# Kernel tuning notes

Measured on AMD Instinct MI355X. Metric: run time of the kernel, lower is better.

The kernel has to match this reference:

```python
import math
import jax, jax.numpy as jnp
import numpy as np

B, S, H, N = 2, 2048, 2048, 16
HN = H // N
ALPHA = 32.0
MASK_VALUE = 10000.0


def setup_inputs() -> dict:
    key = jax.random.key(0)
    k1, k2, k3, k4, k5 = jax.random.split(key, 5)
    hidden_states = jax.random.normal(k1, (B, S, H), dtype=jnp.float32)
    # causal (left-to-right) multiplicative mask, broadcastable to [b, n, s, s]
    ltor_mask = jnp.tril(jnp.ones((S, S), dtype=jnp.float32))[None, None, :, :]
    # torch Linear params: y = x @ W.T + b
    w_qkv = jax.random.normal(k2, (3 * H, H), dtype=jnp.float32) * (1.0 / math.sqrt(H))
    b_qkv = jnp.zeros((3 * H,), dtype=jnp.float32)
    w_dense = jax.random.normal(k3, (H, H), dtype=jnp.float32) * (1.0 / math.sqrt(H))
    b_dense = jnp.zeros((H,), dtype=jnp.float32)
    return {"hidden_states": hidden_states, "ltor_mask": ltor_mask,
            "w_qkv": w_qkv, "b_qkv": b_qkv, "w_dense": w_dense, "b_dense": b_dense}


def reference(hidden_states, ltor_mask, w_qkv, b_qkv, w_dense, b_dense):
    b, s, h = hidden_states.shape
    # fused qkv projection
    qkv = hidden_states @ w_qkv.T + b_qkv                       # [b, s, 3h]
    q, k, v = jnp.split(qkv, 3, axis=-1)

    def heads(t):  # [b, s, h] -> [b, n, s, hn]
        return t.reshape(b, s, N, HN).transpose(0, 2, 1, 3)

    q, k, v = heads(q), heads(k), heads(v)
    # cogview pb_relax: scale query before matmul
    scores = jnp.einsum('bnsd,bntd->bnst', q / math.sqrt(HN), k)  # [b, n, s, s]
    m = ltor_mask[:, :, -s:]
    scores = scores * m - MASK_VALUE * (1.0 - m)
    # pb_relax max stabilization: per (batch, head) global max of scores/alpha
    scaled = scores / ALPHA
    maxes = jax.lax.stop_gradient(jnp.max(scaled, axis=(-2, -1), keepdims=True))
    scores = (scaled - maxes) * ALPHA
    probs = jax.nn.softmax(scores, axis=-1)
    ctx = jnp.einsum('bnst,bntd->bnsd', probs, v)                # [b, n, s, hn]
    ctx = ctx.transpose(0, 2, 1, 3).reshape(b, s, h)
    out = ctx @ w_dense.T + b_dense
    return out
```

## Files before the change

kernel.cpp:

```cpp
#include <hip/hip_runtime.h>

typedef __bf16 bf16_t;
typedef __bf16 bf16x8 __attribute__((ext_vector_type(8)));
typedef __bf16 bf16x4 __attribute__((ext_vector_type(4)));
typedef float f32x4 __attribute__((ext_vector_type(4)));

#define MFMA16(a, b, c) __builtin_amdgcn_mfma_f32_16x16x32_bf16((a), (b), (c), 0, 0, 0)

__device__ __forceinline__ void gload_lds16(const void* g, void* l) {
  __builtin_amdgcn_global_load_lds(
      (__attribute__((address_space(1))) void*)(g),
      (__attribute__((address_space(3))) void*)(l), 16, 0, 0);
}

__device__ __forceinline__ void block_bar() {
  asm volatile("" ::: "memory");
  __builtin_amdgcn_s_barrier();
  asm volatile("" ::: "memory");
}

__global__ __launch_bounds__(256) void cvt_f32_bf16(const float* __restrict__ in,
                                                    bf16_t* __restrict__ out, int n4) {
  int i = blockIdx.x * 256 + threadIdx.x;
  if (i >= n4) return;
  float4 v = ((const float4*)in)[i];
  bf16x4 o;
  o[0] = (bf16_t)v.x; o[1] = (bf16_t)v.y; o[2] = (bf16_t)v.z; o[3] = (bf16_t)v.w;
  ((bf16x4*)out)[i] = o;
}

__global__ __launch_bounds__(512) void gemm_qkv_256(
    const bf16_t* __restrict__ A, const bf16_t* __restrict__ Bw,
    const float* __restrict__ bias,
    bf16_t* __restrict__ qb, bf16_t* __restrict__ kb, bf16_t* __restrict__ vtb,
    int M, int N, int K) {
  __shared__ __attribute__((aligned(16))) bf16_t As[2][256][64];
  __shared__ __attribute__((aligned(16))) bf16_t Bs[2][256][64];
  const int tid = threadIdx.x;
  const int lane = tid & 63;
  const int w = tid >> 6;
  const int wm = w >> 2, wn = w & 3;
  const int l15 = lane & 15, l4 = lane >> 4;
  const int bm = blockIdx.y * 256, bn = blockIdx.x * 256;

  f32x4 acc[8][4];
#pragma unroll
  for (int i = 0; i < 8; ++i)
#pragma unroll
    for (int j = 0; j < 4; ++j)
#pragma unroll
      for (int r = 0; r < 4; ++r) acc[i][j][r] = 0.0f;

  const int srow = tid >> 3;
  const int schk = tid & 7;

  auto stageA = [&](int q, int ti, int i) {
    int r = (i << 6) + srow;
    int cl = (schk ^ (r & 7)) << 3;
    gload_lds16(A + (size_t)(bm + r) * K + (ti << 6) + cl, &As[q][r][schk << 3]);
  };
  auto stageB = [&](int q, int ti, int i) {
    int r = (i << 6) + srow;
    int cl = (schk ^ (r & 7)) << 3;
    gload_lds16(Bw + (size_t)(bn + r) * K + (ti << 6) + cl, &Bs[q][r][schk << 3]);
  };
  auto afrag = [&](int p, int mf, int ks) -> bf16x8 {
    int row = wm * 128 + mf * 16 + l15;
    int ch = ((ks << 2) | l4) ^ (row & 7);
    return *(const bf16x8*)(&As[p][row][ch << 3]);
  };
  auto bfrag = [&](int p, int nf, int ks) -> bf16x8 {
    int row = wn * 64 + nf * 16 + l15;
    int ch = ((ks << 2) | l4) ^ (row & 7);
    return *(const bf16x8*)(&Bs[p][row][ch << 3]);
  };

  const int nt = K >> 6;

#pragma unroll
  for (int i = 0; i < 4; ++i) stageA(0, 0, i);
#pragma unroll
  for (int i = 0; i < 4; ++i) stageB(0, 0, i);

  bf16x8 afr[4], bfr[4];

#pragma unroll 1
  for (int t = 0; t < nt; ++t) {
    const int p = t & 1, q = p ^ 1;
    const bool pf = (t + 1 < nt);
    asm volatile("s_waitcnt vmcnt(0)" ::: "memory");
    block_bar();

#pragma unroll
    for (int n = 0; n < 4; ++n) bfr[n] = bfrag(p, n, 0);
#pragma unroll
    for (int j = 0; j < 4; ++j) afr[j] = afrag(p, j, 0);
    if (pf) { stageA(q, t + 1, 0); stageA(q, t + 1, 1); }
    block_bar();
    __builtin_amdgcn_s_setprio(1);
#pragma unroll
    for (int j = 0; j < 4; ++j)
#pragma unroll
      for (int n = 0; n < 4; ++n) acc[j][n] = MFMA16(afr[j], bfr[n], acc[j][n]);
    __builtin_amdgcn_s_setprio(0);
    block_bar();

#pragma unroll
    for (int j = 0; j < 4; ++j) afr[j] = afrag(p, 4 + j, 0);
    if (pf) { stageA(q, t + 1, 2); stageA(q, t + 1, 3); }
    block_bar();
    __builtin_amdgcn_s_setprio(1);
#pragma unroll
    for (int j = 0; j < 4; ++j)
#pragma unroll
      for (int n = 0; n < 4; ++n) acc[4 + j][n] = MFMA16(afr[j], bfr[n], acc[4 + j][n]);
    __builtin_amdgcn_s_setprio(0);
    block_bar();

#pragma unroll
    for (int n = 0; n < 4; ++n) bfr[n] = bfrag(p, n, 1);
#pragma unroll
    for (int j = 0; j < 4; ++j) afr[j] = afrag(p, j, 1);
    if (pf) { stageB(q, t + 1, 0); stageB(q, t + 1, 1); }
    block_bar();
    __builtin_amdgcn_s_setprio(1);
#pragma unroll
    for (int j = 0; j < 4; ++j)
#pragma unroll
      for (int n = 0; n < 4; ++n) acc[j][n] = MFMA16(afr[j], bfr[n], acc[j][n]);
    __builtin_amdgcn_s_setprio(0);
    block_bar();

#pragma unroll
    for (int j = 0; j < 4; ++j) afr[j] = afrag(p, 4 + j, 1);
    if (pf) { stageB(q, t + 1, 2); stageB(q, t + 1, 3); }
    block_bar();
    __builtin_amdgcn_s_setprio(1);
#pragma unroll
    for (int j = 0; j < 4; ++j)
#pragma unroll
      for (int n = 0; n < 4; ++n) acc[4 + j][n] = MFMA16(afr[j], bfr[n], acc[4 + j][n]);
    __builtin_amdgcn_s_setprio(0);
    block_bar();
  }

  const int which = bn >> 11;
#pragma unroll
  for (int mf = 0; mf < 8; ++mf)
#pragma unroll
    for (int nf = 0; nf < 4; ++nf)
#pragma unroll
      for (int r = 0; r < 4; ++r) {
        int m = bm + wm * 128 + mf * 16 + l4 * 4 + r;
        int n = bn + wn * 64 + nf * 16 + l15;
        float v = acc[mf][nf][r] + bias[n];
        int b = m >> 11, s = m & 2047;
        int d = n & 127;
        int head = (n & 2047) >> 7;
        size_t hb = (size_t)(b * 16 + head);
        if (which == 0) {
          v *= 0.08838834764831845f;
          qb[(hb * 2048 + s) * 128 + d] = (bf16_t)v;
        } else if (which == 1) {
          kb[(hb * 2048 + s) * 128 + d] = (bf16_t)v;
        } else {
          vtb[(hb * 128 + d) * 2048 + s] = (bf16_t)v;
        }
      }
}

__global__ __launch_bounds__(256) void gemm_bt_dense(
    const bf16_t* __restrict__ A, const bf16_t* __restrict__ Bw,
    const float* __restrict__ bias, float* __restrict__ O,
    int M, int N, int K) {
  __shared__ __attribute__((aligned(16))) bf16_t As[2][128][32];
  __shared__ __attribute__((aligned(16))) bf16_t Bs[2][128][32];
  const int tid = threadIdx.x;
  const int lane = tid & 63, wave = tid >> 6;
  const int wr = (wave >> 1) * 64, wc = (wave & 1) * 64;
  const int l15 = lane & 15, l4 = lane >> 4;
  const int bm = blockIdx.y * 128, bn = blockIdx.x * 128;

  f32x4 acc[4][4];
#pragma unroll
  for (int i = 0; i < 4; ++i)
#pragma unroll
    for (int j = 0; j < 4; ++j)
#pragma unroll
      for (int r = 0; r < 4; ++r) acc[i][j][r] = 0.0f;

  const int r0 = tid >> 2;
  const int co = (tid & 3) * 8;
  const bf16_t* gA = A + (size_t)(bm + r0) * K + co;
  const bf16_t* gB = Bw + (size_t)(bn + r0) * K + co;

  const int nt = K >> 5;

  gload_lds16(gA, &As[0][r0][co]);
  gload_lds16(gA + (size_t)64 * K, &As[0][r0 + 64][co]);
  gload_lds16(gB, &Bs[0][r0][co]);
  gload_lds16(gB + (size_t)64 * K, &Bs[0][r0 + 64][co]);

#pragma unroll 1
  for (int t = 0; t < nt; ++t) {
    const int cb = t & 1;
    if (t + 1 < nt) {
      const int kk = (t + 1) << 5;
      const int nb = cb ^ 1;
      gload_lds16(gA + kk, &As[nb][r0][co]);
      gload_lds16(gA + kk + (size_t)64 * K, &As[nb][r0 + 64][co]);
      gload_lds16(gB + kk, &Bs[nb][r0][co]);
      gload_lds16(gB + kk + (size_t)64 * K, &Bs[nb][r0 + 64][co]);
      asm volatile("s_waitcnt vmcnt(4)" ::: "memory");
    } else {
      asm volatile("s_waitcnt vmcnt(0)" ::: "memory");
    }
    block_bar();
    bf16x8 a[4], b[4];
#pragma unroll
    for (int i = 0; i < 4; ++i) a[i] = *(const bf16x8*)(&As[cb][wr + i * 16 + l15][l4 * 8]);
#pragma unroll
    for (int j = 0; j < 4; ++j) b[j] = *(const bf16x8*)(&Bs[cb][wc + j * 16 + l15][l4 * 8]);
#pragma unroll
    for (int i = 0; i < 4; ++i)
#pragma unroll
      for (int j = 0; j < 4; ++j) acc[i][j] = MFMA16(a[i], b[j], acc[i][j]);
    block_bar();
  }

#pragma unroll
  for (int i = 0; i < 4; ++i)
#pragma unroll
    for (int j = 0; j < 4; ++j)
#pragma unroll
      for (int r = 0; r < 4; ++r) {
        int m = bm + wr + i * 16 + l4 * 4 + r;
        int n = bn + wc + j * 16 + l15;
        O[(size_t)m * N + n] = acc[i][j][r] + bias[n];
      }
}

__global__ __launch_bounds__(512) void attn_kernel(
    const bf16_t* __restrict__ qbuf, const bf16_t* __restrict__ kbuf,
    const bf16_t* __restrict__ vtbuf, bf16_t* __restrict__ ctx) {
  __shared__ __attribute__((aligned(16))) bf16_t Ks[2][64][128];
  __shared__ __attribute__((aligned(16))) bf16_t Vts[2][128][64];
  __shared__ __attribute__((aligned(16))) bf16_t Ps[8][16][64];

  const int tid = threadIdx.x, lane = tid & 63, w = tid >> 6;
  const int l15 = lane & 15, l4 = lane >> 4;
  const int hb = blockIdx.y;
  const size_t hoff = (size_t)hb * 2048 * 128;
  const bf16_t* qh = qbuf + hoff;
  const bf16_t* kh = kbuf + hoff;
  const bf16_t* vh = vtbuf + hoff;
  const int b = hb >> 4, head = hb & 15;

  const int kr0 = tid >> 4, ks0 = tid & 15;
  const int vr0 = tid >> 3, vs0 = tid & 7;

  int buf = 0;

#pragma unroll 1
  for (int phase = 0; phase < 2; ++phase) {
    const int qt = phase == 0 ? blockIdx.x : 15 - blockIdx.x;
    const int q0 = qt * 128;
    const int nt = 2 * qt + 2;

    bf16x8 qa[4];
#pragma unroll
    for (int ks = 0; ks < 4; ++ks)
      qa[ks] = *(const bf16x8*)(qh + (size_t)(q0 + w * 16 + l15) * 128 + ks * 32 + l4 * 8);

    f32x4 accO[8];
#pragma unroll
    for (int df = 0; df < 8; ++df)
#pragma unroll
      for (int r = 0; r < 4; ++r) accO[df][r] = 0.0f;
    float mrow[4], lrow[4];
#pragma unroll
    for (int r = 0; r < 4; ++r) { mrow[r] = -1e30f; lrow[r] = 0.0f; }

    {
      const int kv0 = 0;
#pragma unroll
      for (int it = 0; it < 2; ++it) {
        int row = kr0 + it * 32, sch = ks0 ^ (row & 7);
        gload_lds16(kh + (size_t)(kv0 + row) * 128 + sch * 8, &Ks[buf][row][ks0 * 8]);
      }
#pragma unroll
      for (int it = 0; it < 2; ++it) {
        int row = vr0 + it * 64, sch = vs0 ^ (row & 7);
        gload_lds16(vh + (size_t)row * 2048 + kv0 + sch * 8, &Vts[buf][row][vs0 * 8]);
      }
    }

#pragma unroll 1
    for (int t = 0; t < nt; ++t) {
      const int kv0 = t * 64;
      if (t + 1 < nt) {
        const int kvn = (t + 1) * 64;
        const int nb = buf ^ 1;
#pragma unroll
        for (int it = 0; it < 2; ++it) {
          int row = kr0 + it * 32, sch = ks0 ^ (row & 7);
          gload_lds16(kh + (size_t)(kvn + row) * 128 + sch * 8, &Ks[nb][row][ks0 * 8]);
        }
#pragma unroll
        for (int it = 0; it < 2; ++it) {
          int row = vr0 + it * 64, sch = vs0 ^ (row & 7);
          gload_lds16(vh + (size_t)row * 2048 + kvn + sch * 8, &Vts[nb][row][vs0 * 8]);
        }
        asm volatile("s_waitcnt vmcnt(4)" ::: "memory");
      } else {
        asm volatile("s_waitcnt vmcnt(0)" ::: "memory");
      }
      block_bar();

      const bool active = (kv0 <= q0 + w * 16 + 15);
      if (active) {
        f32x4 sc[4];
#pragma unroll
        for (int nf = 0; nf < 4; ++nf) {
#pragma unroll
          for (int r = 0; r < 4; ++r) sc[nf][r] = 0.0f;
          int row = nf * 16 + l15;
#pragma unroll
          for (int ks = 0; ks < 4; ++ks) {
            int ch = (ks * 4 + l4) ^ (row & 7);
            bf16x8 kf = *(const bf16x8*)(&Ks[buf][row][ch * 8]);
            sc[nf] = MFMA16(qa[ks], kf, sc[nf]);
          }
        }

        if (kv0 + 63 > q0 + w * 16) {
#pragma unroll
          for (int nf = 0; nf < 4; ++nf)
#pragma unroll
            for (int r = 0; r < 4; ++r) {
              int qi = q0 + w * 16 + l4 * 4 + r;
              int kv = kv0 + nf * 16 + l15;
              if (kv > qi) sc[nf][r] = -1e30f;
            }
        }

        float tmax[4];
#pragma unroll
        for (int r = 0; r < 4; ++r)
          tmax[r] = fmaxf(fmaxf(sc[0][r], sc[1][r]), fmaxf(sc[2][r], sc[3][r]));
#pragma unroll
        for (int msk = 1; msk <= 8; msk <<= 1)
#pragma unroll
          for (int r = 0; r < 4; ++r)
            tmax[r] = fmaxf(tmax[r], __shfl_xor(tmax[r], msk, 64));

        bool defer = __all(tmax[0] <= mrow[0] + 8.0f && tmax[1] <= mrow[1] + 8.0f &&
                           tmax[2] <= mrow[2] + 8.0f && tmax[3] <= mrow[3] + 8.0f);
        if (!defer) {
          float scl[4];
#pragma unroll
          for (int r = 0; r < 4; ++r) {
            float mn = fmaxf(mrow[r], tmax[r]);
            scl[r] = __expf(mrow[r] - mn);
            mrow[r] = mn;
            lrow[r] *= scl[r];
          }
#pragma unroll
          for (int df = 0; df < 8; ++df)
#pragma unroll
            for (int r = 0; r < 4; ++r) accO[df][r] *= scl[r];
        }

        float rsum[4];
#pragma unroll
        for (int r = 0; r < 4; ++r) {
          float s0 = 0.0f;
#pragma unroll
          for (int nf = 0; nf < 4; ++nf) {
            float p = __expf(sc[nf][r] - mrow[r]);
            sc[nf][r] = p;
            s0 += p;
          }
          rsum[r] = s0;
        }
#pragma unroll
        for (int msk = 1; msk <= 8; msk <<= 1)
#pragma unroll
          for (int r = 0; r < 4; ++r) rsum[r] += __shfl_xor(rsum[r], msk, 64);
#pragma unroll
        for (int r = 0; r < 4; ++r) lrow[r] += rsum[r];

#pragma unroll
        for (int nf = 0; nf < 4; ++nf)
#pragma unroll
          for (int r = 0; r < 4; ++r) {
            int qi = l4 * 4 + r;
            int kv = nf * 16 + l15;
            int ch = (kv >> 3) ^ (qi & 7);
            Ps[w][qi][ch * 8 + (kv & 7)] = (bf16_t)sc[nf][r];
          }

        bf16x8 pa[2];
#pragma unroll
        for (int k2 = 0; k2 < 2; ++k2) {
          int ch = (k2 * 4 + l4) ^ (l15 & 7);
          pa[k2] = *(const bf16x8*)(&Ps[w][l15][ch * 8]);
        }
#pragma unroll
        for (int df = 0; df < 8; ++df) {
          int row = df * 16 + l15;
#pragma unroll
          for (int k2 = 0; k2 < 2; ++k2) {
            int ch = (k2 * 4 + l4) ^ (row & 7);
            bf16x8 vf = *(const bf16x8*)(&Vts[buf][row][ch * 8]);
            accO[df] = MFMA16(pa[k2], vf, accO[df]);
          }
        }
      }
      block_bar();
      buf ^= 1;
    }

    float inv[4];
#pragma unroll
    for (int r = 0; r < 4; ++r) inv[r] = 1.0f / lrow[r];
#pragma unroll
    for (int df = 0; df < 8; ++df)
#pragma unroll
      for (int r = 0; r < 4; ++r) {
        int s = q0 + w * 16 + l4 * 4 + r;
        int col = head * 128 + df * 16 + l15;
        ctx[((size_t)(b * 2048 + s)) * 2048 + col] = (bf16_t)(accO[df][r] * inv[r]);
      }
  }
}

extern "C" void kernel_launch(void* const* d_in, const int* in_sizes, int n_in,
                              void* d_out, int out_size, void* d_ws, size_t ws_size,
                              hipStream_t stream) {
  const float* hs = (const float*)d_in[0];
  const float* w_qkv = (const float*)d_in[2];
  const float* b_qkv = (const float*)d_in[3];
  const float* w_dense = (const float*)d_in[4];
  const float* b_dense = (const float*)d_in[5];
  float* out = (float*)d_out;

  const size_t SZ_HS = (size_t)4096 * 2048;
  const size_t SZ_WQKV = (size_t)6144 * 2048;
  const size_t SZ_WD = (size_t)2048 * 2048;
  const size_t SZ_H = (size_t)32 * 2048 * 128;

  char* ws = (char*)d_ws;
  bf16_t* A_ = (bf16_t*)ws;
  bf16_t* B_ = (bf16_t*)(ws + 2 * SZ_HS);
  bf16_t* Q_ = (bf16_t*)(ws + 2 * (SZ_HS + SZ_WQKV));
  bf16_t* K_ = Q_ + SZ_H;
  bf16_t* V_ = K_ + SZ_H;

  cvt_f32_bf16<<<(int)(SZ_HS / 4 / 256), 256, 0, stream>>>(hs, A_, (int)(SZ_HS / 4));
  cvt_f32_bf16<<<(int)(SZ_WQKV / 4 / 256), 256, 0, stream>>>(w_qkv, B_, (int)(SZ_WQKV / 4));

  gemm_qkv_256<<<dim3(24, 16), 512, 0, stream>>>(A_, B_, b_qkv, Q_, K_, V_, 4096, 6144, 2048);

  cvt_f32_bf16<<<(int)(SZ_WD / 4 / 256), 256, 0, stream>>>(w_dense, A_, (int)(SZ_WD / 4));

  attn_kernel<<<dim3(8, 32), 512, 0, stream>>>(Q_, K_, V_, B_);

  gemm_bt_dense<<<dim3(16, 32), 256, 0, stream>>>(B_, A_, b_dense, out, 4096, 2048, 2048);
}
```

Before: 440.2 us.

## Use triple-buffered K=32 stages in QKV GEMM with fewer barriers

```diff
diff --git a/kernel.cpp b/kernel.cpp
--- a/kernel.cpp
+++ b/kernel.cpp
@@ -34,8 +34,8 @@
     const float* __restrict__ bias,
     bf16_t* __restrict__ qb, bf16_t* __restrict__ kb, bf16_t* __restrict__ vtb,
     int M, int N, int K) {
-  __shared__ __attribute__((aligned(16))) bf16_t As[2][256][64];
-  __shared__ __attribute__((aligned(16))) bf16_t Bs[2][256][64];
+  __shared__ __attribute__((aligned(16))) bf16_t As[3][256][32];
+  __shared__ __attribute__((aligned(16))) bf16_t Bs[3][256][32];
   const int tid = threadIdx.x;
   const int lane = tid & 63;
   const int w = tid >> 6;
@@ -51,90 +51,70 @@
 #pragma unroll
       for (int r = 0; r < 4; ++r) acc[i][j][r] = 0.0f;
 
-  const int srow = tid >> 3;
-  const int schk = tid & 7;
+  const int srow = tid >> 2;
+  const int schk = tid & 3;
 
   auto stageA = [&](int q, int ti, int i) {
-    int r = (i << 6) + srow;
-    int cl = (schk ^ (r & 7)) << 3;
-    gload_lds16(A + (size_t)(bm + r) * K + (ti << 6) + cl, &As[q][r][schk << 3]);
+    int r = (i << 7) + srow;
+    int cl = (schk ^ (r & 3)) << 3;
+    gload_lds16(A + (size_t)(bm + r) * K + (ti << 5) + cl, &As[q][r][schk << 3]);
   };
   auto stageB = [&](int q, int ti, int i) {
-    int r = (i << 6) + srow;
-    int cl = (schk ^ (r & 7)) << 3;
-    gload_lds16(Bw + (size_t)(bn + r) * K + (ti << 6) + cl, &Bs[q][r][schk << 3]);
+    int r = (i << 7) + srow;
+    int cl = (schk ^ (r & 3)) << 3;
+    gload_lds16(Bw + (size_t)(bn + r) * K + (ti << 5) + cl, &Bs[q][r][schk << 3]);
   };
-  auto afrag = [&](int p, int mf, int ks) -> bf16x8 {
+  auto afrag = [&](int p, int mf) -> bf16x8 {
     int row = wm * 128 + mf * 16 + l15;
-    int ch = ((ks << 2) | l4) ^ (row & 7);
+    int ch = l4 ^ (row & 3);
     return *(const bf16x8*)(&As[p][row][ch << 3]);
   };
-  auto bfrag = [&](int p, int nf, int ks) -> bf16x8 {
+  auto bfrag = [&](int p, int nf) -> bf16x8 {
     int row = wn * 64 + nf * 16 + l15;
-    int ch = ((ks << 2) | l4) ^ (row & 7);
+    int ch = l4 ^ (row & 3);
     return *(const bf16x8*)(&Bs[p][row][ch << 3]);
   };
 
-  const int nt = K >> 6;
-
-#pragma unroll
-  for (int i = 0; i < 4; ++i) stageA(0, 0, i);
-#pragma unroll
-  for (int i = 0; i < 4; ++i) stageB(0, 0, i);
-
-  bf16x8 afr[4], bfr[4];
+  const int nt = K >> 5;
+
+#pragma unroll
+  for (int i = 0; i < 2; ++i) stageA(0, 0, i);
+#pragma unroll
+  for (int i = 0; i < 2; ++i) stageB(0, 0, i);
+#pragma unroll
+  for (int i = 0; i < 2; ++i) stageA(1, 1, i);
+#pragma unroll
+  for (int i = 0; i < 2; ++i) stageB(1, 1, i);
 
 #pragma unroll 1
   for (int t = 0; t < nt; ++t) {
-    const int p = t & 1, q = p ^ 1;
-    const bool pf = (t + 1 < nt);
-    asm volatile("s_waitcnt vmcnt(0)" ::: "memory");
+    const int sl = t % 3;
+    if (t + 1 < nt) {
+      asm volatile("s_waitcnt vmcnt(4)" ::: "memory");
+    } else {
+      asm volatile("s_waitcnt vmcnt(0)" ::: "memory");
+    }
     block_bar();
 
-#pragma unroll
-    for (int n = 0; n < 4; ++n) bfr[n] = bfrag(p, n, 0);
-#pragma unroll
-    for (int j = 0; j < 4; ++j) afr[j] = afrag(p, j, 0);
-    if (pf) { stageA(q, t + 1, 0); stageA(q, t + 1, 1); }
-    block_bar();
+    const bool pf = (t + 2 < nt);
+    const int s2 = pf ? (t + 2) % 3 : 0;
+
+    bf16x8 bfr[4], afr[4];
+#pragma unroll
+    for (int n = 0; n < 4; ++n) bfr[n] = bfrag(sl, n);
+#pragma unroll
+    for (int j = 0; j < 4; ++j) afr[j] = afrag(sl, j);
+    if (pf) { stageA(s2, t + 2, 0); stageA(s2, t + 2, 1); }
     __builtin_amdgcn_s_setprio(1);
 #pragma unroll
     for (int j = 0; j < 4; ++j)
 #pragma unroll
       for (int n = 0; n < 4; ++n) acc[j][n] = MFMA16(afr[j], bfr[n], acc[j][n]);
     __builtin_amdgcn_s_setprio(0);
-    block_bar();
-
-#pragma unroll
-    for (int j = 0; j < 4; ++j) afr[j] = afrag(p, 4 + j, 0);
-    if (pf) { stageA(q, t + 1, 2); stageA(q, t + 1, 3); }
-    block_bar();
-    __builtin_amdgcn_s_setprio(1);
-#pragma unroll
-    for (int j = 0; j < 4; ++j)
-#pragma unroll
-      for (int n = 0; n < 4; ++n) acc[4 + j][n] = MFMA16(afr[j], bfr[n], acc[4 + j][n]);
-    __builtin_amdgcn_s_setprio(0);
-    block_bar();
-
-#pragma unroll
-    for (int n = 0; n < 4; ++n) bfr[n] = bfrag(p, n, 1);
-#pragma unroll
-    for (int j = 0; j < 4; ++j) afr[j] = afrag(p, j, 1);
-    if (pf) { stageB(q, t + 1, 0); stageB(q, t + 1, 1); }
-    block_bar();
-    __builtin_amdgcn_s_setprio(1);
-#pragma unroll
-    for (int j = 0; j < 4; ++j)
-#pragma unroll
-      for (int n = 0; n < 4; ++n) acc[j][n] = MFMA16(afr[j], bfr[n], acc[j][n]);
-    __builtin_amdgcn_s_setprio(0);
-    block_bar();
-
-#pragma unroll
-    for (int j = 0; j < 4; ++j) afr[j] = afrag(p, 4 + j, 1);
-    if (pf) { stageB(q, t + 1, 2); stageB(q, t + 1, 3); }
-    block_bar();
+
+#pragma unroll
+    for (int j = 0; j < 4; ++j) afr[j] = afrag(sl, 4 + j);
+    if (pf) { stageB(s2, t + 2, 0); stageB(s2, t + 2, 1); }
     __builtin_amdgcn_s_setprio(1);
 #pragma unroll
     for (int j = 0; j < 4; ++j)
```

After: 431.4 us. 1.02x faster.
